# Performance work log

Measured on AMD Instinct MI355X. Metric: run time of the kernel, lower is better.

## Reference

```python
import jax, jax.numpy as jnp
import numpy as np

NUM_EMBEDDINGS = 1024
EMBEDDING_DIM = 256
COMMITMENT_COST = 0.25


def setup_inputs() -> dict:
    key = jax.random.key(0)
    k_z, k_e = jax.random.split(key)
    z = jax.random.normal(k_z, (16, EMBEDDING_DIM, 4096), dtype=jnp.float32)
    # nn.Embedding init: uniform(-1/K, 1/K)
    emb = jax.random.uniform(
        k_e, (NUM_EMBEDDINGS, EMBEDDING_DIM), dtype=jnp.float32,
        minval=-1.0 / NUM_EMBEDDINGS, maxval=1.0 / NUM_EMBEDDINGS)
    return {"z": z, "emb": emb}


def reference(z, emb):
    # z: [B, D, T] -> [B, T, D]
    zt = jnp.transpose(z, (0, 2, 1))
    B, T, D = zt.shape
    flat = zt.reshape(-1, D)  # [N, D]
    dists = (jnp.sum(flat * flat, axis=1, keepdims=True)
             + jnp.sum(emb * emb, axis=1)
             - 2.0 * jnp.matmul(flat, emb.T))
    idx = jnp.argmin(dists, axis=1)          # [N]
    quantized = emb[idx].reshape(B, T, D)    # gather + reshape
    e_latent_loss = jnp.mean((jax.lax.stop_gradient(quantized) - zt) ** 2)
    q_latent_loss = jnp.mean((quantized - jax.lax.stop_gradient(zt)) ** 2)
    loss = q_latent_loss + COMMITMENT_COST * e_latent_loss
    # straight-through estimator
    quantized_st = zt + jax.lax.stop_gradient(quantized - zt)
    return jnp.transpose(quantized_st, (0, 2, 1)), loss
```

## Files before the change

kernel.cpp:

```cpp
#include <hip/hip_runtime.h>
#include <stdint.h>

#define B_   16
#define D_   256
#define T_   4096
#define K_   1024
#define N_   (B_ * T_)
#define BM   64
#define NKT  64

typedef __attribute__((ext_vector_type(4))) float floatx4;
typedef __attribute__((ext_vector_type(2))) float floatx2;

__global__ __launch_bounds__(256) void emb_prep(const float* __restrict__ emb,
                                                uint32_t* __restrict__ embf8,
                                                float* __restrict__ esqh,
                                                float* __restrict__ lossp) {
    int w = threadIdx.x >> 6, lane = threadIdx.x & 63;
    int k = blockIdx.x * 4 + w;
    float4 v = ((const float4*)emb)[k * 64 + lane];
    float a0 = v.x * 1024.f, a1 = v.y * 1024.f, a2 = v.z * 1024.f, a3 = v.w * 1024.f;
    int p = __builtin_amdgcn_cvt_pk_fp8_f32(a0, a1, 0, false);
    p = __builtin_amdgcn_cvt_pk_fp8_f32(a2, a3, p, true);
    embf8[k * 64 + lane] = (uint32_t)p;
    float ss = a0 * a0 + a1 * a1 + a2 * a2 + a3 * a3;
    #pragma unroll
    for (int off = 32; off; off >>= 1) ss += __shfl_xor(ss, off, 64);
    if (lane == 0) esqh[k] = ss * (0.5f / 1024.f);
    if (blockIdx.x == 0 && threadIdx.x == 0) *lossp = 0.f;
}

__global__ __launch_bounds__(256, 4) void vq_main(const float* __restrict__ z,
                                                  const uint32_t* __restrict__ embf8,
                                                  const float* __restrict__ esqh,
                                                  float* __restrict__ out0,
                                                  float* __restrict__ lossp) {
    __shared__ __align__(16) unsigned char xs[BM * 256];
    __shared__ __align__(16) unsigned char es[2][16 * 256];
    __shared__ int   pidx[BM];
    __shared__ float lred[4];

    int tid  = threadIdx.x;
    int lane = tid & 63, w = tid >> 6;
    int ml   = lane & 15, quad = lane >> 4;
    int blk  = blockIdx.x;
    int b    = blk >> 6;
    int t0   = (blk & 63) * BM;
    const float* zb = z + (size_t)b * (D_ * T_) + t0;

    {
        int t = lane;
        int hf = (t >> 4) & 1;
        #pragma unroll 2
        for (int j = 0; j < 8; ++j) {
            int dgrp = w + 4 * j;
            int d0 = dgrp * 8;
            float f0 = zb[(d0 + 0) * T_ + t];
            float f1 = zb[(d0 + 1) * T_ + t];
            float f2 = zb[(d0 + 2) * T_ + t];
            float f3 = zb[(d0 + 3) * T_ + t];
            float f4 = zb[(d0 + 4) * T_ + t];
            float f5 = zb[(d0 + 5) * T_ + t];
            float f6 = zb[(d0 + 6) * T_ + t];
            float f7 = zb[(d0 + 7) * T_ + t];
            uint32_t p0 = (uint32_t)__builtin_amdgcn_cvt_pk_fp8_f32(f0, f1, 0, false);
            p0 = (uint32_t)__builtin_amdgcn_cvt_pk_fp8_f32(f2, f3, (int)p0, true);
            uint32_t p1 = (uint32_t)__builtin_amdgcn_cvt_pk_fp8_f32(f4, f5, 0, false);
            p1 = (uint32_t)__builtin_amdgcn_cvt_pk_fp8_f32(f6, f7, (int)p1, true);
            int c = dgrp >> 1, h = dgrp & 1;
            int off = ((c ^ (t & 15)) << 4) + ((h ^ hf) << 3);
            *(uint2*)&xs[t * 256 + off] = make_uint2(p0, p1);
        }
    }
    __syncthreads();

    long afr[8];
    {
        int p = w * 16 + ml;
        int flip = w & 1;
        #pragma unroll
        for (int kk = 0; kk < 8; ++kk) {
            int c = 2 * kk + (quad >> 1), h = quad & 1;
            int off = ((c ^ ml) << 4) + ((h ^ flip) << 3);
            afr[kk] = *(const long*)&xs[p * 256 + off];
        }
    }

    int eoff[8];
    #pragma unroll
    for (int kk = 0; kk < 8; ++kk) {
        int c = 2 * kk + (quad >> 1), h = quad & 1;
        eoff[kk] = ml * 256 + ((c ^ ml) << 4) + (h << 3);
    }
    const int eswoff = (tid >> 4) * 256 + (((tid & 15) ^ (tid >> 4)) << 4);

    *(uint4*)&es[0][eswoff] = ((const uint4*)embf8)[tid];
    uint4 r0 = ((const uint4*)embf8)[256 + tid];
    __syncthreads();

    float bv[4]; int bi[4];
    #pragma unroll
    for (int i = 0; i < 4; ++i) { bv[i] = 1e30f; bi[i] = 0; }

    #pragma unroll 2
    for (int kt = 0; kt < NKT; ++kt) {
        int cur = kt & 1;
        if (kt + 1 < NKT) *(uint4*)&es[cur ^ 1][eswoff] = r0;
        if (kt + 2 < NKT) r0 = ((const uint4*)embf8)[(kt + 2) * 256 + tid];
        float eh = esqh[kt * 16 + ml];
        floatx4 acc = {0.f, 0.f, 0.f, 0.f};
        #pragma unroll
        for (int kk = 0; kk < 8; ++kk) {
            long bf = *(const long*)&es[cur][eoff[kk]];
            acc = __builtin_amdgcn_mfma_f32_16x16x32_fp8_fp8(afr[kk], bf, acc, 0, 0, 0);
        }
        int c = kt * 16 + ml;
        #pragma unroll
        for (int i = 0; i < 4; ++i) {
            float v = eh - acc[i];
            if (v < bv[i]) { bv[i] = v; bi[i] = c; }
        }
        __syncthreads();
    }

    #pragma unroll
    for (int i = 0; i < 4; ++i) {
        float v = bv[i]; int ii = bi[i];
        #pragma unroll
        for (int off = 1; off < 16; off <<= 1) {
            float ov = __shfl_xor(v, off, 64);
            int   oi = __shfl_xor(ii, off, 64);
            if (ov < v || (ov == v && oi < ii)) { v = ov; ii = oi; }
        }
        if (ml == 0) pidx[w * 16 + quad * 4 + i] = ii;
    }
    __syncthreads();

    #pragma unroll
    for (int m = 0; m < 4; ++m) {
        int t   = (tid >> 4) + 16 * m;
        int off = tid & 15;
        int code = pidx[t];
        uint4 v = ((const uint4*)embf8)[code * 16 + off];
        *(uint4*)&xs[t * 256 + ((off ^ (t & 15)) << 4)] = v;
    }
    __syncthreads();

    float lsum = 0.f;
    float* ob = out0 + (size_t)b * (D_ * T_) + t0;
    {
        int t = lane;
        #pragma unroll
        for (int j = 0; j < 4; ++j) {
            int g = w + 4 * j;
            uint4 v = *(const uint4*)&xs[t * 256 + ((g ^ (t & 15)) << 4)];
            uint32_t wd[4] = {v.x, v.y, v.z, v.w};
            #pragma unroll
            for (int u = 0; u < 4; ++u) {
                floatx2 lo = __builtin_amdgcn_cvt_pk_f32_fp8((int)wd[u], false);
                floatx2 hi = __builtin_amdgcn_cvt_pk_f32_fp8((int)wd[u], true);
                float q[4] = {lo[0] * (1.f/1024.f), lo[1] * (1.f/1024.f),
                              hi[0] * (1.f/1024.f), hi[1] * (1.f/1024.f)};
                #pragma unroll
                for (int s = 0; s < 4; ++s) {
                    int d = g * 16 + u * 4 + s;
                    float zv = zb[d * T_ + t];
                    ob[d * T_ + t] = q[s];
                    float df = q[s] - zv;
                    lsum = fmaf(df, df, lsum);
                }
            }
        }
    }
    #pragma unroll
    for (int off = 32; off; off >>= 1) lsum += __shfl_xor(lsum, off, 64);
    if (lane == 0) lred[w] = lsum;
    __syncthreads();
    if (tid == 0)
        atomicAdd(lossp, (lred[0] + lred[1] + lred[2] + lred[3]) * (1.25f / 16777216.0f));
}

extern "C" void kernel_launch(void* const* d_in, const int* in_sizes, int n_in,
                              void* d_out, int out_size, void* d_ws, size_t ws_size,
                              hipStream_t stream) {
    (void)in_sizes; (void)n_in; (void)out_size; (void)ws_size;
    const float* z   = (const float*)d_in[0];
    const float* emb = (const float*)d_in[1];

    uint32_t* embf8 = (uint32_t*)d_ws;
    float*    esqh  = (float*)((char*)d_ws + (size_t)K_ * D_);

    float* out0  = (float*)d_out;
    float* lossp = out0 + (size_t)N_ * D_;

    emb_prep<<<K_ / 4, 256, 0, stream>>>(emb, embf8, esqh, lossp);
    vq_main<<<N_ / BM, 256, 0, stream>>>(z, embf8, esqh, out0, lossp);
}
```

Measured before the change: 148.0 us.

## Stream codebook fragments from global, split K across waves, derive loss algebraically

Drops the LDS double-buffered codebook staging and its per-tile barriers. Each wave now loads its B fragments directly from a pre-permuted fp8 codebook in global memory (L2-resident), handles two 16-row M tiles against half of the codes, and the two code halves are merged through shared memory. The loss is rebuilt from ||z||^2 plus the winning distance value, which removes the second read of z in the epilogue. The tradeoff is that the loss now rests on fp8-quantized dot products, and each wave issues more global loads for the codebook.

```diff
diff --git a/kernel.cpp b/kernel.cpp
--- a/kernel.cpp
+++ b/kernel.cpp
@@ -7,10 +7,10 @@
 #define K_   1024
 #define N_   (B_ * T_)
 #define BM   64
-#define NKT  64
 
 typedef __attribute__((ext_vector_type(4))) float floatx4;
 typedef __attribute__((ext_vector_type(2))) float floatx2;
+typedef __attribute__((ext_vector_type(2))) long longx2;
 
 __global__ __launch_bounds__(256) void emb_prep(const float* __restrict__ emb,
                                                 uint32_t* __restrict__ embf8,
@@ -22,7 +22,8 @@
     float a0 = v.x * 1024.f, a1 = v.y * 1024.f, a2 = v.z * 1024.f, a3 = v.w * 1024.f;
     int p = __builtin_amdgcn_cvt_pk_fp8_f32(a0, a1, 0, false);
     p = __builtin_amdgcn_cvt_pk_fp8_f32(a2, a3, p, true);
-    embf8[k * 64 + lane] = (uint32_t)p;
+    int widx = ((lane >> 1) & 3) * 16 + (lane >> 3) * 2 + (lane & 1);
+    embf8[k * 64 + widx] = (uint32_t)p;
     float ss = a0 * a0 + a1 * a1 + a2 * a2 + a3 * a3;
     #pragma unroll
     for (int off = 32; off; off >>= 1) ss += __shfl_xor(ss, off, 64);
@@ -36,21 +37,23 @@
                                                   float* __restrict__ out0,
                                                   float* __restrict__ lossp) {
     __shared__ __align__(16) unsigned char xs[BM * 256];
-    __shared__ __align__(16) unsigned char es[2][16 * 256];
+    __shared__ float wvals[2][BM];
+    __shared__ int   widx[2][BM];
     __shared__ int   pidx[BM];
-    __shared__ float lred[4];
+    __shared__ float zred[4];
 
     int tid  = threadIdx.x;
     int lane = tid & 63, w = tid >> 6;
     int ml   = lane & 15, quad = lane >> 4;
+    int ph   = w & 1, ch = w >> 1;
     int blk  = blockIdx.x;
     int b    = blk >> 6;
     int t0   = (blk & 63) * BM;
     const float* zb = z + (size_t)b * (D_ * T_) + t0;
 
+    float zsq = 0.f;
     {
-        int t = lane;
-        int hf = (t >> 4) & 1;
+        int t = lane, hf = (t >> 4) & 1;
         #pragma unroll 2
         for (int j = 0; j < 8; ++j) {
             int dgrp = w + 4 * j;
@@ -63,76 +66,95 @@
             float f5 = zb[(d0 + 5) * T_ + t];
             float f6 = zb[(d0 + 6) * T_ + t];
             float f7 = zb[(d0 + 7) * T_ + t];
+            zsq += f0*f0 + f1*f1 + f2*f2 + f3*f3 + f4*f4 + f5*f5 + f6*f6 + f7*f7;
             uint32_t p0 = (uint32_t)__builtin_amdgcn_cvt_pk_fp8_f32(f0, f1, 0, false);
             p0 = (uint32_t)__builtin_amdgcn_cvt_pk_fp8_f32(f2, f3, (int)p0, true);
             uint32_t p1 = (uint32_t)__builtin_amdgcn_cvt_pk_fp8_f32(f4, f5, 0, false);
             p1 = (uint32_t)__builtin_amdgcn_cvt_pk_fp8_f32(f6, f7, (int)p1, true);
             int c = dgrp >> 1, h = dgrp & 1;
-            int off = ((c ^ (t & 15)) << 4) + ((h ^ hf) << 3);
-            *(uint2*)&xs[t * 256 + off] = make_uint2(p0, p1);
-        }
-    }
-    __syncthreads();
-
-    long afr[8];
-    {
-        int p = w * 16 + ml;
-        int flip = w & 1;
+            *(uint2*)&xs[t * 256 + ((c ^ (t & 15)) << 4) + ((h ^ hf) << 3)] =
+                make_uint2(p0, p1);
+        }
+    }
+    __syncthreads();
+
+    long afr[2][8];
+    #pragma unroll
+    for (int s = 0; s < 2; ++s) {
+        int p = (ph * 2 + s) * 16 + ml;
         #pragma unroll
         for (int kk = 0; kk < 8; ++kk) {
             int c = 2 * kk + (quad >> 1), h = quad & 1;
-            int off = ((c ^ ml) << 4) + ((h ^ flip) << 3);
-            afr[kk] = *(const long*)&xs[p * 256 + off];
-        }
-    }
-
-    int eoff[8];
-    #pragma unroll
-    for (int kk = 0; kk < 8; ++kk) {
-        int c = 2 * kk + (quad >> 1), h = quad & 1;
-        eoff[kk] = ml * 256 + ((c ^ ml) << 4) + (h << 3);
-    }
-    const int eswoff = (tid >> 4) * 256 + (((tid & 15) ^ (tid >> 4)) << 4);
-
-    *(uint4*)&es[0][eswoff] = ((const uint4*)embf8)[tid];
-    uint4 r0 = ((const uint4*)embf8)[256 + tid];
-    __syncthreads();
-
-    float bv[4]; int bi[4];
-    #pragma unroll
-    for (int i = 0; i < 4; ++i) { bv[i] = 1e30f; bi[i] = 0; }
-
+            afr[s][kk] = *(const long*)&xs[p * 256 + ((c ^ ml) << 4) + ((h ^ s) << 3)];
+        }
+    }
+
+    float bv[2][4]; int bi[2][4];
+    #pragma unroll
+    for (int s = 0; s < 2; ++s)
+        #pragma unroll
+        for (int i = 0; i < 4; ++i) { bv[s][i] = 1e30f; bi[s][i] = 0; }
+
+    const char* eb = (const char*)embf8;
     #pragma unroll 2
-    for (int kt = 0; kt < NKT; ++kt) {
-        int cur = kt & 1;
-        if (kt + 1 < NKT) *(uint4*)&es[cur ^ 1][eswoff] = r0;
-        if (kt + 2 < NKT) r0 = ((const uint4*)embf8)[(kt + 2) * 256 + tid];
-        float eh = esqh[kt * 16 + ml];
-        floatx4 acc = {0.f, 0.f, 0.f, 0.f};
+    for (int j = 0; j < 32; ++j) {
+        int kt = ch * 32 + j;
+        int c  = kt * 16 + ml;
+        const longx2* brow = (const longx2*)(eb + (size_t)c * 256 + quad * 64);
+        longx2 q0 = brow[0], q1 = brow[1], q2 = brow[2], q3 = brow[3];
+        float eh = esqh[c];
+        floatx4 acc0 = {0.f, 0.f, 0.f, 0.f};
+        floatx4 acc1 = {0.f, 0.f, 0.f, 0.f};
+        long bf[8] = {q0[0], q0[1], q1[0], q1[1], q2[0], q2[1], q3[0], q3[1]};
         #pragma unroll
         for (int kk = 0; kk < 8; ++kk) {
-            long bf = *(const long*)&es[cur][eoff[kk]];
-            acc = __builtin_amdgcn_mfma_f32_16x16x32_fp8_fp8(afr[kk], bf, acc, 0, 0, 0);
-        }
-        int c = kt * 16 + ml;
+            acc0 = __builtin_amdgcn_mfma_f32_16x16x32_fp8_fp8(afr[0][kk], bf[kk], acc0, 0, 0, 0);
+            acc1 = __builtin_amdgcn_mfma_f32_16x16x32_fp8_fp8(afr[1][kk], bf[kk], acc1, 0, 0, 0);
+        }
         #pragma unroll
         for (int i = 0; i < 4; ++i) {
-            float v = eh - acc[i];
-            if (v < bv[i]) { bv[i] = v; bi[i] = c; }
-        }
-        __syncthreads();
-    }
-
-    #pragma unroll
-    for (int i = 0; i < 4; ++i) {
-        float v = bv[i]; int ii = bi[i];
-        #pragma unroll
-        for (int off = 1; off < 16; off <<= 1) {
-            float ov = __shfl_xor(v, off, 64);
-            int   oi = __shfl_xor(ii, off, 64);
-            if (ov < v || (ov == v && oi < ii)) { v = ov; ii = oi; }
-        }
-        if (ml == 0) pidx[w * 16 + quad * 4 + i] = ii;
+            float v0 = eh - acc0[i];
+            if (v0 < bv[0][i]) { bv[0][i] = v0; bi[0][i] = c; }
+            float v1 = eh - acc1[i];
+            if (v1 < bv[1][i]) { bv[1][i] = v1; bi[1][i] = c; }
+        }
+    }
+
+    #pragma unroll
+    for (int s = 0; s < 2; ++s)
+        #pragma unroll
+        for (int i = 0; i < 4; ++i) {
+            float v = bv[s][i]; int ii = bi[s][i];
+            #pragma unroll
+            for (int off = 1; off < 16; off <<= 1) {
+                float ov = __shfl_xor(v, off, 64);
+                int   oi = __shfl_xor(ii, off, 64);
+                if (ov < v || (ov == v && oi < ii)) { v = ov; ii = oi; }
+            }
+            if (ml == 0) {
+                int pt = (ph * 2 + s) * 16 + quad * 4 + i;
+                wvals[ch][pt] = v; widx[ch][pt] = ii;
+            }
+        }
+    #pragma unroll
+    for (int off = 32; off; off >>= 1) zsq += __shfl_xor(zsq, off, 64);
+    if (lane == 0) zred[w] = zsq;
+    __syncthreads();
+
+    if (tid < 64) {
+        int t = tid;
+        float v0 = wvals[0][t]; int i0 = widx[0][t];
+        float v1 = wvals[1][t]; int i1 = widx[1][t];
+        float wv = v0; int wi = i0;
+        if (v1 < v0 || (v1 == v0 && i1 < i0)) { wv = v1; wi = i1; }
+        pidx[t] = wi;
+        float lsum = wv;
+        #pragma unroll
+        for (int off = 32; off; off >>= 1) lsum += __shfl_xor(lsum, off, 64);
+        if (t == 0) {
+            float tot = zred[0] + zred[1] + zred[2] + zred[3] + lsum * (2.0f / 1024.f);
+            atomicAdd(lossp, tot * (1.25f / 16777216.0f));
+        }
     }
     __syncthreads();
 
@@ -146,7 +168,6 @@
     }
     __syncthreads();
 
-    float lsum = 0.f;
     float* ob = out0 + (size_t)b * (D_ * T_) + t0;
     {
         int t = lane;
@@ -157,27 +178,17 @@
             uint32_t wd[4] = {v.x, v.y, v.z, v.w};
             #pragma unroll
             for (int u = 0; u < 4; ++u) {
+                int kk = (g & 3) * 2 + (u >> 1);
+                int d0 = kk * 32 + (g >> 2) * 8 + (u & 1) * 4;
                 floatx2 lo = __builtin_amdgcn_cvt_pk_f32_fp8((int)wd[u], false);
                 floatx2 hi = __builtin_amdgcn_cvt_pk_f32_fp8((int)wd[u], true);
-                float q[4] = {lo[0] * (1.f/1024.f), lo[1] * (1.f/1024.f),
-                              hi[0] * (1.f/1024.f), hi[1] * (1.f/1024.f)};
-                #pragma unroll
-                for (int s = 0; s < 4; ++s) {
-                    int d = g * 16 + u * 4 + s;
-                    float zv = zb[d * T_ + t];
-                    ob[d * T_ + t] = q[s];
-                    float df = q[s] - zv;
-                    lsum = fmaf(df, df, lsum);
-                }
+                ob[(d0 + 0) * T_ + t] = lo[0] * (1.f / 1024.f);
+                ob[(d0 + 1) * T_ + t] = lo[1] * (1.f / 1024.f);
+                ob[(d0 + 2) * T_ + t] = hi[0] * (1.f / 1024.f);
+                ob[(d0 + 3) * T_ + t] = hi[1] * (1.f / 1024.f);
             }
         }
     }
-    #pragma unroll
-    for (int off = 32; off; off >>= 1) lsum += __shfl_xor(lsum, off, 64);
-    if (lane == 0) lred[w] = lsum;
-    __syncthreads();
-    if (tid == 0)
-        atomicAdd(lossp, (lred[0] + lred[1] + lred[2] + lred[3]) * (1.25f / 16777216.0f));
 }
 
 extern "C" void kernel_launch(void* const* d_in, const int* in_sizes, int n_in,
```

After: 174.4 us. +17.8%, slower.
